# Kernel tuning notes

Measured on AMD Instinct MI355X. Metric: run time of the kernel, lower is better.

## Reference

```python
import jax, jax.numpy as jnp
import numpy as np
from jax import lax

B, W, M = 4, 20, 512
RNN_HID = 64
N_HIDDEN = RNN_HID          # bi = False
HALF = N_HIDDEN // 2
K = 10
LONG_K = W // 2             # conv_long kernel
LONG_OUT = W - 2 * (LONG_K - 1)   # = 2
N_SPATIAL = 10


def setup_inputs() -> dict:
    key = jax.random.key(0)
    ks = jax.random.split(key, 24)
    g = lambda i, shape, s=0.05: jax.random.normal(ks[i], shape, jnp.float32) * s
    return {
        "x": jax.random.normal(ks[0], (B, W, M), jnp.float32),
        # vanilla RNN (tanh), 1 layer, input_size=1
        "W_ih": g(1, (RNN_HID, 1), 0.2), "W_hh": g(2, (RNN_HID, RNN_HID), 0.1),
        "b_ih": g(3, (RNN_HID,)), "b_hh": g(4, (RNN_HID,)),
        # attention adjacency params
        "W1": g(5, (HALF, N_HIDDEN), 0.1), "b1": g(6, (HALF,)),
        "W2": g(7, (HALF, N_HIDDEN), 0.1),
        "V": g(8, (HALF,), 0.1), "bv": g(9, (1,)),
        "Wb": g(10, (M, M), 0.05), "wb": g(11, (1,)),
        # conv / conv_long
        "conv_w": g(12, (K, 1, W), 0.1), "conv_b": g(13, (K,)),
        "convl_w": g(14, (K, 1, LONG_K), 0.1), "convl_b": g(15, (K,)),
        # graph conv layers: adj @ (x @ W) + b
        "gc1_w": g(16, ((1 + LONG_OUT) * K, N_HIDDEN), 0.1), "gc1_b": g(17, (N_HIDDEN,)),
        "gc2_w": g(18, (N_HIDDEN, N_SPATIAL), 0.1), "gc2_b": g(19, (N_SPATIAL,)),
        # output head
        "out_w": g(20, (1, N_HIDDEN + N_SPATIAL), 0.1), "out_b": g(21, (1,)),
        # fixed geographic adjacency (data.adj)
        "adj": jax.random.uniform(ks[22], (M, M), dtype=jnp.float32),
    }


def _conv1d(x, w, b, dilation=1):
    # x: (N, Cin, W), w: (Cout, Cin, K) -> (N, Cout, Wout), VALID padding
    y = lax.conv_general_dilated(x, w, (1,), 'VALID', rhs_dilation=(dilation,),
                                 dimension_numbers=('NCH', 'OIH', 'NCH'))
    return y + b[None, :, None]


def reference(x, W_ih, W_hh, b_ih, b_hh, W1, b1, W2, V, bv, Wb, wb,
              conv_w, conv_b, convl_w, convl_b, gc1_w, gc1_b, gc2_w, gc2_b,
              out_w, out_b, adj):
    b, w, m = x.shape
    # ---- RNN encode each node's scalar series: (b*m, w, 1) -> last hidden ----
    xr = jnp.transpose(x, (0, 2, 1)).reshape(b * m, w)          # (bm, w)
    inp = xr[..., None] @ W_ih.T + b_ih                         # (bm, w, H)

    def step(h, u):
        return jnp.tanh(u + h @ W_hh.T + b_hh), None

    h0 = jnp.zeros((b * m, RNN_HID), x.dtype)
    h_last, _ = lax.scan(step, h0, jnp.swapaxes(inp, 0, 1))     # (bm, H)
    last_hid = h_last.reshape(b, m, N_HIDDEN)
    out_temporal = last_hid

    # ---- pairwise bilinear attention adjacency (broadcast instead of repeat) ----
    p = last_hid @ W1.T                                         # (b, m, H/2)
    q = last_hid @ W2.T                                         # (b, m, H/2)
    e = jax.nn.elu(p[:, :, None, :] + q[:, None, :, :] + b1)    # (b, m, m, H/2)
    a_mx = e @ V + bv[0]                                        # (b, m, m)
    # F.normalize(p=2, dim=1)
    nrm = jnp.maximum(jnp.sqrt(jnp.sum(a_mx * a_mx, axis=1, keepdims=True)), 1e-12)
    a_mx = a_mx / nrm
    c = jax.nn.sigmoid(a_mx @ Wb + wb[0])                       # (b, m, m)
    A = adj[None] * c + a_mx * (1.0 - c)

    # ---- per-node convs, batched over all b*m series (no Python loop) ----
    h_tmp = xr[:, None, :]                                      # (bm, 1, w)
    r = _conv1d(h_tmp, conv_w, conv_b)                          # (bm, k, 1)
    r_long = _conv1d(h_tmp, convl_w, convl_b, dilation=2)       # (bm, k, long_out)
    r_l = jnp.concatenate([r, r_long], axis=-1).reshape(b, m, -1)  # (b, m, (1+lo)*k)
    r_l = jax.nn.relu(r_l)

    # ---- graph convolutions: adj @ (x @ W) + b ----
    xg = jax.nn.relu(A @ (r_l @ gc1_w) + gc1_b)                 # (b, m, H)
    out_spatial = jax.nn.relu(A @ (xg @ gc2_w) + gc2_b)         # (b, m, 10)

    out = jnp.concatenate([out_spatial, out_temporal], axis=-1)
    return (out @ out_w.T + out_b)[..., 0]                      # (b, m)
```

## Files before the change

kernel.cpp:

```cpp
#include <hip/hip_runtime.h>
#include <hip/hip_bf16.h>
#include <cstdint>
#include <cstddef>

#define OFF_P     0
#define OFF_QB    65536
#define OFF_TDOT  131072
#define OFF_COLSQ 133120
#define OFF_ZT    135168
#define OFF_AMXB  155648
#define OFF_ABF   679936
#define OFF_G1T   1204224

typedef __attribute__((ext_vector_type(8))) short short8;
typedef __attribute__((ext_vector_type(8))) unsigned short ushort8;
typedef __attribute__((ext_vector_type(4))) float f32x4;

__device__ inline unsigned short f2bf(float f) {
    unsigned u = __builtin_bit_cast(unsigned, f);
    unsigned r = u + 0x7FFFu + ((u >> 16) & 1u);
    return (unsigned short)(r >> 16);
}
__device__ inline float bf2f(unsigned short s) {
    unsigned u = ((unsigned)s) << 16;
    return __builtin_bit_cast(float, u);
}
__device__ inline float tanh_fast(float x) {
    return 1.f - 2.f/(__expf(2.f*x) + 1.f);
}

__global__ __launch_bounds__(256) void k1_rnn(
    const float* __restrict__ x, const float* __restrict__ W_ih,
    const float* __restrict__ W_hh, const float* __restrict__ b_ih,
    const float* __restrict__ b_hh, const float* __restrict__ W1,
    const float* __restrict__ b1, const float* __restrict__ W2,
    const float* __restrict__ conv_w, const float* __restrict__ conv_b,
    const float* __restrict__ convl_w, const float* __restrict__ convl_b,
    const float* __restrict__ gc1_w, const float* __restrict__ out_w,
    const float* __restrict__ out_b,
    float* __restrict__ p_out, float* __restrict__ qb_out,
    unsigned short* __restrict__ G1T, float* __restrict__ tdot,
    float* __restrict__ colsq)
{
    __shared__ float h_sh[4][64];
    __shared__ float xt_sh[4][20];
    __shared__ float rl_sh[4][30];
    int tid = threadIdx.x;
    int w = tid >> 6, lane = tid & 63;
    int s = blockIdx.x * 4 + w;
    int b = s >> 9, m = s & 511;

    if (blockIdx.x < 8) colsq[blockIdx.x * 256 + tid] = 0.f;

    if (lane < 20) xt_sh[w][lane] = x[(b*20 + lane)*512 + m];

    float wrow[64];
    const float* wr = W_hh + lane*64;
    #pragma unroll
    for (int k4 = 0; k4 < 16; ++k4) {
        float4 v = reinterpret_cast<const float4*>(wr)[k4];
        wrow[4*k4+0]=v.x; wrow[4*k4+1]=v.y; wrow[4*k4+2]=v.z; wrow[4*k4+3]=v.w;
    }
    float wih = W_ih[lane], bih = b_ih[lane], bhh = b_hh[lane];
    h_sh[w][lane] = 0.f;
    float h = 0.f;

    if (lane < 10) {
        float acc = conv_b[lane];
        #pragma unroll
        for (int t = 0; t < 20; ++t) acc += conv_w[lane*20+t]*xt_sh[w][t];
        rl_sh[w][3*lane] = fmaxf(acc, 0.f);
    } else if (lane < 30) {
        int idx = lane-10, j = idx>>1, oo = idx&1;
        float acc = convl_b[j];
        #pragma unroll
        for (int t = 0; t < 10; ++t) acc += convl_w[j*10+t]*xt_sh[w][oo+2*t];
        rl_sh[w][3*j+1+oo] = fmaxf(acc, 0.f);
    }

    for (int t = 0; t < 20; ++t) {
        float acc = xt_sh[w][t]*wih + bih + bhh;
        #pragma unroll
        for (int k = 0; k < 64; ++k) acc += wrow[k]*h_sh[w][k];
        h = tanh_fast(acc);
        h_sh[w][lane] = h;
    }

    float td = h * out_w[10 + lane];
    #pragma unroll
    for (int off = 32; off; off >>= 1) td += __shfl_down(td, off);
    if (lane == 0) tdot[s] = td + out_b[0];

    if (lane < 32) {
        const float* w1r = W1 + lane*64;
        float acc = 0.f;
        #pragma unroll
        for (int k = 0; k < 64; ++k) acc += w1r[k]*h_sh[w][k];
        p_out[s*32 + lane] = acc;
    } else {
        int i = lane - 32;
        const float* w2r = W2 + i*64;
        float acc = 0.f;
        #pragma unroll
        for (int k = 0; k < 64; ++k) acc += w2r[k]*h_sh[w][k];
        qb_out[s*32 + i] = acc + b1[i];
    }

    float g = 0.f;
    #pragma unroll
    for (int t = 0; t < 30; ++t) g += rl_sh[w][t]*gc1_w[t*64 + lane];
    G1T[((size_t)(b*64 + lane))*512 + m] = f2bf(g);
}

__global__ __launch_bounds__(256) void k2_amx(
    const float* __restrict__ p, const float* __restrict__ qb,
    const float* __restrict__ V, const float* __restrict__ bv,
    unsigned short* __restrict__ amxB, float* __restrict__ colsq)
{
    __shared__ float p_sh[32*36], q_sh[32*36], v_sh[32], sq_sh[32*17];
    int t = threadIdx.x;
    int b = blockIdx.z, i0 = blockIdx.y*32, j0 = blockIdx.x*32;
    {
        int r = t >> 3, c4 = (t & 7)*4;
        *(float4*)&p_sh[r*36 + c4] = *(const float4*)(p  + (size_t)(b*512 + i0 + r)*32 + c4);
        *(float4*)&q_sh[r*36 + c4] = *(const float4*)(qb + (size_t)(b*512 + j0 + r)*32 + c4);
    }
    if (t < 32) v_sh[t] = V[t];
    __syncthreads();

    int ti = t >> 4, tj = t & 15;
    float bv0 = bv[0];
    float a00 = bv0, a01 = bv0, a10 = bv0, a11 = bv0;
    #pragma unroll
    for (int h = 0; h < 32; ++h) {
        float p0 = p_sh[ti*36 + h], p1 = p_sh[(ti+16)*36 + h];
        float q0 = q_sh[tj*36 + h], q1 = q_sh[(tj+16)*36 + h];
        float vh = v_sh[h];
        float x00 = p0+q0, x01 = p0+q1, x10 = p1+q0, x11 = p1+q1;
        float e00 = x00 > 0.f ? x00 : __expf(x00)-1.f;
        float e01 = x01 > 0.f ? x01 : __expf(x01)-1.f;
        float e10 = x10 > 0.f ? x10 : __expf(x10)-1.f;
        float e11 = x11 > 0.f ? x11 : __expf(x11)-1.f;
        a00 += vh*e00; a01 += vh*e01; a10 += vh*e10; a11 += vh*e11;
    }
    size_t base0 = ((size_t)(b*512 + i0 + ti))*512 + j0;
    size_t base1 = ((size_t)(b*512 + i0 + ti + 16))*512 + j0;
    amxB[base0 + tj]      = f2bf(a00);
    amxB[base0 + tj + 16] = f2bf(a01);
    amxB[base1 + tj]      = f2bf(a10);
    amxB[base1 + tj + 16] = f2bf(a11);

    sq_sh[tj*17 + ti]      = a00*a00 + a10*a10;
    sq_sh[(tj+16)*17 + ti] = a01*a01 + a11*a11;
    __syncthreads();
    if (t < 32) {
        float ssum = 0.f;
        #pragma unroll
        for (int r = 0; r < 16; ++r) ssum += sq_sh[t*17 + r];
        atomicAdd(&colsq[b*512 + j0 + t], ssum);
    }
}

__global__ __launch_bounds__(64) void k3a_mfma(
    const unsigned short* __restrict__ amxB, const float* __restrict__ Wb,
    const float* __restrict__ colsq, const float* __restrict__ wb,
    const float* __restrict__ adj, unsigned short* __restrict__ Abf)
{
    int lane = threadIdx.x;
    int b = blockIdx.z;
    int i0 = blockIdx.y*32, j0 = blockIdx.x*32;
    f32x4 acc[2][2] = {};

    int kslice = (lane>>4)*8;
    int fr = lane & 15;
    const unsigned short* abase = amxB + ((size_t)(b*512 + i0 + fr))*512 + kslice;
    const float* wcol = Wb + j0 + fr;
    const float* csq  = colsq + b*512 + kslice;

    for (int k0 = 0; k0 < 512; k0 += 32) {
        float4 c0 = *(const float4*)(csq + k0);
        float4 c1 = *(const float4*)(csq + k0 + 4);
        float inv[8] = {
            rsqrtf(fmaxf(c0.x,1e-24f)), rsqrtf(fmaxf(c0.y,1e-24f)),
            rsqrtf(fmaxf(c0.z,1e-24f)), rsqrtf(fmaxf(c0.w,1e-24f)),
            rsqrtf(fmaxf(c1.x,1e-24f)), rsqrtf(fmaxf(c1.y,1e-24f)),
            rsqrtf(fmaxf(c1.z,1e-24f)), rsqrtf(fmaxf(c1.w,1e-24f)) };

        short8 a0 = *(const short8*)(abase + k0);
        short8 a1 = *(const short8*)(abase + 16*512 + k0);

        const float* wk = wcol + (size_t)(k0 + kslice)*512;
        short8 b0, b1;
        #pragma unroll
        for (int m = 0; m < 8; ++m) {
            b0[m] = (short)f2bf(wk[(size_t)m*512]      * inv[m]);
            b1[m] = (short)f2bf(wk[(size_t)m*512 + 16] * inv[m]);
        }

        acc[0][0] = __builtin_amdgcn_mfma_f32_16x16x32_bf16(a0, b0, acc[0][0],0,0,0);
        acc[0][1] = __builtin_amdgcn_mfma_f32_16x16x32_bf16(a0, b1, acc[0][1],0,0,0);
        acc[1][0] = __builtin_amdgcn_mfma_f32_16x16x32_bf16(a1, b0, acc[1][0],0,0,0);
        acc[1][1] = __builtin_amdgcn_mfma_f32_16x16x32_bf16(a1, b1, acc[1][1],0,0,0);
    }

    float wbs = wb[0];
    #pragma unroll
    for (int fj = 0; fj < 2; ++fj) {
        int j = j0 + fj*16 + fr;
        float inv = rsqrtf(fmaxf(colsq[b*512 + j], 1e-24f));
        #pragma unroll
        for (int fi = 0; fi < 2; ++fi)
        #pragma unroll
        for (int r = 0; r < 4; ++r) {
            int i = i0 + fi*16 + (lane>>4)*4 + r;
            float S = acc[fi][fj][r] + wbs;
            float c = 1.f/(1.f + __expf(-S));
            float aN = bf2f(amxB[((size_t)(b*512)+i)*512 + j]) * inv;
            Abf[((size_t)(b*512)+i)*512 + j] = f2bf(adj[i*512+j]*c + aN*(1.f - c));
        }
    }
}

#define AS_STRIDE 520
__global__ __launch_bounds__(256) void k3b_mfma(
    const unsigned short* __restrict__ Abf, const unsigned short* __restrict__ G1T,
    const float* __restrict__ gc1_b, const float* __restrict__ gc2_w,
    float* __restrict__ zT)
{
    __shared__ __align__(16) unsigned short As[16*AS_STRIDE];
    __shared__ float xg[16][68];
    int t = threadIdx.x;
    int b = blockIdx.y, i0 = blockIdx.x*16;
    int wv = t >> 6, lane = t & 63;

    {
        int r = t >> 4, seg = (t & 15)*32;
        const unsigned short* src = Abf + ((size_t)(b*512 + i0 + r))*512 + seg;
        *(short8*)&As[r*AS_STRIDE + seg]      = *(const short8*)src;
        *(short8*)&As[r*AS_STRIDE + seg + 8]  = *(const short8*)(src + 8);
        *(short8*)&As[r*AS_STRIDE + seg + 16] = *(const short8*)(src + 16);
        *(short8*)&As[r*AS_STRIDE + seg + 24] = *(const short8*)(src + 24);
    }
    __syncthreads();

    f32x4 acc = {};
    const unsigned short* gbase = G1T + ((size_t)(b*64 + wv*16 + (lane&15)))*512 + (lane>>4)*8;
    int aoff = (lane&15)*AS_STRIDE + (lane>>4)*8;
    #pragma unroll 4
    for (int k0 = 0; k0 < 512; k0 += 32) {
        short8 af = *(const short8*)&As[aoff + k0];
        short8 bf = *(const short8*)(gbase + k0);
        acc = __builtin_amdgcn_mfma_f32_16x16x32_bf16(af, bf, acc, 0,0,0);
    }

    {
        int cc = wv*16 + (lane&15);
        float gb = gc1_b[cc];
        #pragma unroll
        for (int r = 0; r < 4; ++r)
            xg[(lane>>4)*4 + r][cc] = fmaxf(acc[r] + gb, 0.f);
    }
    __syncthreads();

    if (t < 160) {
        int row = t/10, sx = t%10;
        float a = 0.f;
        #pragma unroll
        for (int c = 0; c < 64; ++c) a += xg[row][c]*gc2_w[c*10 + sx];
        zT[((size_t)(b*10) + sx)*512 + i0 + row] = a;
    }
}

__global__ __launch_bounds__(256) void k4_out(
    const unsigned short* __restrict__ Abf, const float* __restrict__ zT,
    const float* __restrict__ gc2_b, const float* __restrict__ out_w,
    const float* __restrict__ tdot, float* __restrict__ out)
{
    int t = threadIdx.x;
    int w = t >> 6, lane = t & 63;
    int s = blockIdx.x*4 + w;
    int b = s >> 9;

    short8 av = *(const short8*)(Abf + (size_t)s*512 + lane*8);
    float a[8];
    #pragma unroll
    for (int q = 0; q < 8; ++q) a[q] = bf2f((unsigned short)av[q]);

    float acc[10];
    #pragma unroll
    for (int sx = 0; sx < 10; ++sx) {
        const float* zr = zT + ((size_t)(b*10) + sx)*512 + lane*8;
        float4 z0 = *(const float4*)zr;
        float4 z1 = *(const float4*)(zr + 4);
        acc[sx] = a[0]*z0.x + a[1]*z0.y + a[2]*z0.z + a[3]*z0.w
                + a[4]*z1.x + a[5]*z1.y + a[6]*z1.z + a[7]*z1.w;
    }
    #pragma unroll
    for (int sx = 0; sx < 10; ++sx)
        #pragma unroll
        for (int off = 32; off; off >>= 1) acc[sx] += __shfl_down(acc[sx], off);
    if (lane == 0) {
        float o = tdot[s];
        #pragma unroll
        for (int sx = 0; sx < 10; ++sx)
            o += fmaxf(acc[sx] + gc2_b[sx], 0.f) * out_w[sx];
        out[s] = o;
    }
}

extern "C" void kernel_launch(void* const* d_in, const int* in_sizes, int n_in,
                              void* d_out, int out_size, void* d_ws, size_t ws_size,
                              hipStream_t stream) {
    const float* x       = (const float*)d_in[0];
    const float* W_ih    = (const float*)d_in[1];
    const float* W_hh    = (const float*)d_in[2];
    const float* b_ih    = (const float*)d_in[3];
    const float* b_hh    = (const float*)d_in[4];
    const float* W1      = (const float*)d_in[5];
    const float* b1      = (const float*)d_in[6];
    const float* W2      = (const float*)d_in[7];
    const float* V       = (const float*)d_in[8];
    const float* bv      = (const float*)d_in[9];
    const float* Wb      = (const float*)d_in[10];
    const float* wb      = (const float*)d_in[11];
    const float* conv_w  = (const float*)d_in[12];
    const float* conv_b  = (const float*)d_in[13];
    const float* convl_w = (const float*)d_in[14];
    const float* convl_b = (const float*)d_in[15];
    const float* gc1_w   = (const float*)d_in[16];
    const float* gc1_b   = (const float*)d_in[17];
    const float* gc2_w   = (const float*)d_in[18];
    const float* gc2_b   = (const float*)d_in[19];
    const float* out_w   = (const float*)d_in[20];
    const float* out_b   = (const float*)d_in[21];
    const float* adj     = (const float*)d_in[22];

    float* ws    = (float*)d_ws;
    float* p     = ws + OFF_P;
    float* qb    = ws + OFF_QB;
    float* tdot  = ws + OFF_TDOT;
    float* colsq = ws + OFF_COLSQ;
    float* zT    = ws + OFF_ZT;
    unsigned short* amxB = (unsigned short*)(ws + OFF_AMXB);
    unsigned short* Abf  = (unsigned short*)(ws + OFF_ABF);
    unsigned short* G1T  = (unsigned short*)(ws + OFF_G1T);
    float* out   = (float*)d_out;

    k1_rnn<<<dim3(512), dim3(256), 0, stream>>>(
        x, W_ih, W_hh, b_ih, b_hh, W1, b1, W2,
        conv_w, conv_b, convl_w, convl_b, gc1_w, out_w, out_b,
        p, qb, G1T, tdot, colsq);

    k2_amx<<<dim3(16,16,4), dim3(256), 0, stream>>>(p, qb, V, bv, amxB, colsq);

    k3a_mfma<<<dim3(16,16,4), dim3(64), 0, stream>>>(amxB, Wb, colsq, wb, adj, Abf);
    k3b_mfma<<<dim3(32,4), dim3(256), 0, stream>>>(Abf, G1T, gc1_b, gc2_w, zT);
    k4_out<<<dim3(512), dim3(256), 0, stream>>>(Abf, zT, gc2_b, out_w, tdot, out);
}
```

Baseline: 59.42 us.

## Fuse gate GEMM with first graph-conv GEMM and pre-transpose Wb to bf16

Merges k3a and k3b into one kernel. Each block loads a 16-row strip of the attention matrix, normalizes it once into LDS, computes the gate GEMM against a bf16 transposed Wb, writes the blended adjacency to both global memory and LDS, then runs the G1 GEMM straight from LDS. Wb is transposed and converted to bf16 in extra blocks of the RNN kernel. This removes one launch, re-reading Abf, and the per-k fp32 Wb conversion inside the MFMA loop. The cost is only 128 blocks doing a full 16x512x512 GEMM each, which lowers parallelism. Normalization is now applied to A in bf16 rather than folded into the fp32 B operand, so rounding changes slightly.

```diff
diff --git a/kernel.cpp b/kernel.cpp
--- a/kernel.cpp
+++ b/kernel.cpp
@@ -11,6 +11,7 @@
 #define OFF_AMXB  155648
 #define OFF_ABF   679936
 #define OFF_G1T   1204224
+#define OFF_WBT   1269760
 
 typedef __attribute__((ext_vector_type(8))) short short8;
 typedef __attribute__((ext_vector_type(8))) unsigned short ushort8;
@@ -37,15 +38,40 @@
     const float* __restrict__ conv_w, const float* __restrict__ conv_b,
     const float* __restrict__ convl_w, const float* __restrict__ convl_b,
     const float* __restrict__ gc1_w, const float* __restrict__ out_w,
-    const float* __restrict__ out_b,
+    const float* __restrict__ out_b, const float* __restrict__ Wb,
     float* __restrict__ p_out, float* __restrict__ qb_out,
     unsigned short* __restrict__ G1T, float* __restrict__ tdot,
-    float* __restrict__ colsq)
+    float* __restrict__ colsq, unsigned short* __restrict__ WbT)
 {
     __shared__ float h_sh[4][64];
     __shared__ float xt_sh[4][20];
     __shared__ float rl_sh[4][30];
+    __shared__ float tile[64][68];
     int tid = threadIdx.x;
+
+    if (blockIdx.x >= 512) {
+        int tt = blockIdx.x - 512;
+        int k0 = (tt >> 3) * 64, j0 = (tt & 7) * 64;
+        #pragma unroll
+        for (int q = 0; q < 4; ++q) {
+            int kr = (tid>>4) + 16*q;
+            int jc = (tid&15)*4;
+            *(float4*)&tile[kr][jc] = *(const float4*)(Wb + (size_t)(k0+kr)*512 + j0 + jc);
+        }
+        __syncthreads();
+        int jl = tid>>2, kc = (tid&3)*16;
+        int j = j0 + jl;
+        ushort8 v0, v1;
+        #pragma unroll
+        for (int kk = 0; kk < 8; ++kk) v0[kk] = f2bf(tile[kc+kk][jl]);
+        #pragma unroll
+        for (int kk = 0; kk < 8; ++kk) v1[kk] = f2bf(tile[kc+8+kk][jl]);
+        unsigned short* dst = WbT + (size_t)j*512 + k0 + kc;
+        *(ushort8*)dst = v0;
+        *(ushort8*)(dst+8) = v1;
+        return;
+    }
+
     int w = tid >> 6, lane = tid & 63;
     int s = blockIdx.x * 4 + w;
     int b = s >> 9, m = s & 511;
@@ -161,104 +187,90 @@
     }
 }
 
-__global__ __launch_bounds__(64) void k3a_mfma(
-    const unsigned short* __restrict__ amxB, const float* __restrict__ Wb,
-    const float* __restrict__ colsq, const float* __restrict__ wb,
-    const float* __restrict__ adj, unsigned short* __restrict__ Abf)
+#define K3S 520
+__global__ __launch_bounds__(256) void k3_fused(
+    const unsigned short* __restrict__ amxB, const unsigned short* __restrict__ WbT,
+    const unsigned short* __restrict__ G1T, const float* __restrict__ colsq,
+    const float* __restrict__ wb, const float* __restrict__ adj,
+    const float* __restrict__ gc1_b, const float* __restrict__ gc2_w,
+    unsigned short* __restrict__ Abf, float* __restrict__ zT)
 {
-    int lane = threadIdx.x;
-    int b = blockIdx.z;
-    int i0 = blockIdx.y*32, j0 = blockIdx.x*32;
-    f32x4 acc[2][2] = {};
-
-    int kslice = (lane>>4)*8;
-    int fr = lane & 15;
-    const unsigned short* abase = amxB + ((size_t)(b*512 + i0 + fr))*512 + kslice;
-    const float* wcol = Wb + j0 + fr;
-    const float* csq  = colsq + b*512 + kslice;
-
-    for (int k0 = 0; k0 < 512; k0 += 32) {
-        float4 c0 = *(const float4*)(csq + k0);
-        float4 c1 = *(const float4*)(csq + k0 + 4);
-        float inv[8] = {
-            rsqrtf(fmaxf(c0.x,1e-24f)), rsqrtf(fmaxf(c0.y,1e-24f)),
-            rsqrtf(fmaxf(c0.z,1e-24f)), rsqrtf(fmaxf(c0.w,1e-24f)),
-            rsqrtf(fmaxf(c1.x,1e-24f)), rsqrtf(fmaxf(c1.y,1e-24f)),
-            rsqrtf(fmaxf(c1.z,1e-24f)), rsqrtf(fmaxf(c1.w,1e-24f)) };
-
-        short8 a0 = *(const short8*)(abase + k0);
-        short8 a1 = *(const short8*)(abase + 16*512 + k0);
-
-        const float* wk = wcol + (size_t)(k0 + kslice)*512;
-        short8 b0, b1;
-        #pragma unroll
-        for (int m = 0; m < 8; ++m) {
-            b0[m] = (short)f2bf(wk[(size_t)m*512]      * inv[m]);
-            b1[m] = (short)f2bf(wk[(size_t)m*512 + 16] * inv[m]);
-        }
-
-        acc[0][0] = __builtin_amdgcn_mfma_f32_16x16x32_bf16(a0, b0, acc[0][0],0,0,0);
-        acc[0][1] = __builtin_amdgcn_mfma_f32_16x16x32_bf16(a0, b1, acc[0][1],0,0,0);
-        acc[1][0] = __builtin_amdgcn_mfma_f32_16x16x32_bf16(a1, b0, acc[1][0],0,0,0);
-        acc[1][1] = __builtin_amdgcn_mfma_f32_16x16x32_bf16(a1, b1, acc[1][1],0,0,0);
-    }
-
-    float wbs = wb[0];
-    #pragma unroll
-    for (int fj = 0; fj < 2; ++fj) {
-        int j = j0 + fj*16 + fr;
-        float inv = rsqrtf(fmaxf(colsq[b*512 + j], 1e-24f));
-        #pragma unroll
-        for (int fi = 0; fi < 2; ++fi)
-        #pragma unroll
-        for (int r = 0; r < 4; ++r) {
-            int i = i0 + fi*16 + (lane>>4)*4 + r;
-            float S = acc[fi][fj][r] + wbs;
-            float c = 1.f/(1.f + __expf(-S));
-            float aN = bf2f(amxB[((size_t)(b*512)+i)*512 + j]) * inv;
-            Abf[((size_t)(b*512)+i)*512 + j] = f2bf(adj[i*512+j]*c + aN*(1.f - c));
-        }
-    }
-}
-
-#define AS_STRIDE 520
-__global__ __launch_bounds__(256) void k3b_mfma(
-    const unsigned short* __restrict__ Abf, const unsigned short* __restrict__ G1T,
-    const float* __restrict__ gc1_b, const float* __restrict__ gc2_w,
-    float* __restrict__ zT)
-{
-    __shared__ __align__(16) unsigned short As[16*AS_STRIDE];
+    __shared__ float inv_lds[512];
+    __shared__ __align__(16) unsigned short A_lds[16*K3S];
     __shared__ float xg[16][68];
     int t = threadIdx.x;
     int b = blockIdx.y, i0 = blockIdx.x*16;
     int wv = t >> 6, lane = t & 63;
+    int fr = lane & 15, sl = (lane>>4)*8;
+
+    if (t < 128) {
+        float4 c = *(const float4*)(colsq + b*512 + t*4);
+        float4 iv = { rsqrtf(fmaxf(c.x,1e-24f)), rsqrtf(fmaxf(c.y,1e-24f)),
+                      rsqrtf(fmaxf(c.z,1e-24f)), rsqrtf(fmaxf(c.w,1e-24f)) };
+        *(float4*)&inv_lds[t*4] = iv;
+    }
+    __syncthreads();
 
     {
         int r = t >> 4, seg = (t & 15)*32;
-        const unsigned short* src = Abf + ((size_t)(b*512 + i0 + r))*512 + seg;
-        *(short8*)&As[r*AS_STRIDE + seg]      = *(const short8*)src;
-        *(short8*)&As[r*AS_STRIDE + seg + 8]  = *(const short8*)(src + 8);
-        *(short8*)&As[r*AS_STRIDE + seg + 16] = *(const short8*)(src + 16);
-        *(short8*)&As[r*AS_STRIDE + seg + 24] = *(const short8*)(src + 24);
-    }
-    __syncthreads();
-
-    f32x4 acc = {};
-    const unsigned short* gbase = G1T + ((size_t)(b*64 + wv*16 + (lane&15)))*512 + (lane>>4)*8;
-    int aoff = (lane&15)*AS_STRIDE + (lane>>4)*8;
-    #pragma unroll 4
+        const unsigned short* src = amxB + ((size_t)(b*512 + i0 + r))*512 + seg;
+        #pragma unroll
+        for (int q = 0; q < 4; ++q) {
+            short8 v = *(const short8*)(src + q*8);
+            ushort8 o;
+            #pragma unroll
+            for (int e = 0; e < 8; ++e)
+                o[e] = f2bf(bf2f((unsigned short)v[e]) * inv_lds[seg + q*8 + e]);
+            *(ushort8*)&A_lds[r*K3S + seg + q*8] = o;
+        }
+    }
+    __syncthreads();
+
+    f32x4 acc[8] = {};
+    int wj0 = wv*128;
     for (int k0 = 0; k0 < 512; k0 += 32) {
-        short8 af = *(const short8*)&As[aoff + k0];
-        short8 bf = *(const short8*)(gbase + k0);
-        acc = __builtin_amdgcn_mfma_f32_16x16x32_bf16(af, bf, acc, 0,0,0);
-    }
+        short8 a = *(const short8*)&A_lds[fr*K3S + k0 + sl];
+        #pragma unroll
+        for (int fj = 0; fj < 8; ++fj) {
+            short8 bb = *(const short8*)(WbT + ((size_t)(wj0 + fj*16 + fr))*512 + k0 + sl);
+            acc[fj] = __builtin_amdgcn_mfma_f32_16x16x32_bf16(a, bb, acc[fj],0,0,0);
+        }
+    }
+    __syncthreads();
 
     {
-        int cc = wv*16 + (lane&15);
+        float wbs = wb[0];
+        #pragma unroll
+        for (int fj = 0; fj < 8; ++fj) {
+            int j = wj0 + fj*16 + fr;
+            #pragma unroll
+            for (int r = 0; r < 4; ++r) {
+                int i = sl/2 + r;
+                float S = acc[fj][r] + wbs;
+                float c = 1.f/(1.f + __expf(-S));
+                float aN = bf2f(A_lds[i*K3S + j]);
+                unsigned short u = f2bf(adj[(size_t)(i0+i)*512 + j]*c + aN*(1.f - c));
+                Abf[((size_t)(b*512) + i0 + i)*512 + j] = u;
+                A_lds[i*K3S + j] = u;
+            }
+        }
+    }
+    __syncthreads();
+
+    {
+        f32x4 acc2 = {};
+        const unsigned short* gbase = G1T + ((size_t)(b*64 + wv*16 + fr))*512 + sl;
+        #pragma unroll 4
+        for (int k0 = 0; k0 < 512; k0 += 32) {
+            short8 a = *(const short8*)&A_lds[fr*K3S + k0 + sl];
+            short8 g = *(const short8*)(gbase + k0);
+            acc2 = __builtin_amdgcn_mfma_f32_16x16x32_bf16(a, g, acc2,0,0,0);
+        }
+        int cc = wv*16 + fr;
         float gb = gc1_b[cc];
         #pragma unroll
         for (int r = 0; r < 4; ++r)
-            xg[(lane>>4)*4 + r][cc] = fmaxf(acc[r] + gb, 0.f);
+            xg[sl/2 + r][cc] = fmaxf(acc2[r] + gb, 0.f);
     }
     __syncthreads();
 
@@ -344,16 +356,18 @@
     unsigned short* amxB = (unsigned short*)(ws + OFF_AMXB);
     unsigned short* Abf  = (unsigned short*)(ws + OFF_ABF);
     unsigned short* G1T  = (unsigned short*)(ws + OFF_G1T);
+    unsigned short* WbT  = (unsigned short*)(ws + OFF_WBT);
     float* out   = (float*)d_out;
 
-    k1_rnn<<<dim3(512), dim3(256), 0, stream>>>(
+    k1_rnn<<<dim3(576), dim3(256), 0, stream>>>(
         x, W_ih, W_hh, b_ih, b_hh, W1, b1, W2,
-        conv_w, conv_b, convl_w, convl_b, gc1_w, out_w, out_b,
-        p, qb, G1T, tdot, colsq);
+        conv_w, conv_b, convl_w, convl_b, gc1_w, out_w, out_b, Wb,
+        p, qb, G1T, tdot, colsq, WbT);
 
     k2_amx<<<dim3(16,16,4), dim3(256), 0, stream>>>(p, qb, V, bv, amxB, colsq);
 
-    k3a_mfma<<<dim3(16,16,4), dim3(64), 0, stream>>>(amxB, Wb, colsq, wb, adj, Abf);
-    k3b_mfma<<<dim3(32,4), dim3(256), 0, stream>>>(Abf, G1T, gc1_b, gc2_w, zT);
+    k3_fused<<<dim3(32,4), dim3(256), 0, stream>>>(
+        amxB, WbT, G1T, colsq, wb, adj, gc1_b, gc2_w, Abf, zT);
+
     k4_out<<<dim3(512), dim3(256), 0, stream>>>(Abf, zT, gc2_b, out_w, tdot, out);
 }
```

Result: slower. 80.59 us (+35.6%).

## Pre-transpose Wb to bf16 in RNN kernel and apply norm scaling on A side

Applied to the files above, without the earlier changes.

Adds 64 extra blocks to the RNN kernel that transpose Wb into a bf16 k-contiguous layout in workspace. The Wb GEMM kernel then loads B fragments as vectors instead of eight strided fp32 loads with per-element conversion. The column-norm scaling moves onto the amx operand, which is now bf16-decoded, scaled and re-rounded. The RNN recurrence inner product is also split into four accumulators to shorten the dependency chain, at the cost of extra shared-memory use in the RNN kernel and a slightly different rounding path.

```diff
diff --git a/kernel.cpp b/kernel.cpp
--- a/kernel.cpp
+++ b/kernel.cpp
@@ -11,6 +11,7 @@
 #define OFF_AMXB  155648
 #define OFF_ABF   679936
 #define OFF_G1T   1204224
+#define OFF_WBT   1269760
 
 typedef __attribute__((ext_vector_type(8))) short short8;
 typedef __attribute__((ext_vector_type(8))) unsigned short ushort8;
@@ -37,15 +38,40 @@
     const float* __restrict__ conv_w, const float* __restrict__ conv_b,
     const float* __restrict__ convl_w, const float* __restrict__ convl_b,
     const float* __restrict__ gc1_w, const float* __restrict__ out_w,
-    const float* __restrict__ out_b,
+    const float* __restrict__ out_b, const float* __restrict__ Wb,
     float* __restrict__ p_out, float* __restrict__ qb_out,
     unsigned short* __restrict__ G1T, float* __restrict__ tdot,
-    float* __restrict__ colsq)
+    float* __restrict__ colsq, unsigned short* __restrict__ WbT)
 {
     __shared__ float h_sh[4][64];
     __shared__ float xt_sh[4][20];
     __shared__ float rl_sh[4][30];
+    __shared__ float tile[64][68];
     int tid = threadIdx.x;
+
+    if (blockIdx.x >= 512) {
+        int tt = blockIdx.x - 512;
+        int k0 = (tt >> 3) * 64, j0 = (tt & 7) * 64;
+        #pragma unroll
+        for (int q = 0; q < 4; ++q) {
+            int kr = (tid>>4) + 16*q;
+            int jc = (tid&15)*4;
+            *(float4*)&tile[kr][jc] = *(const float4*)(Wb + (size_t)(k0+kr)*512 + j0 + jc);
+        }
+        __syncthreads();
+        int jl = tid>>2, kc = (tid&3)*16;
+        int j = j0 + jl;
+        ushort8 v0, v1;
+        #pragma unroll
+        for (int kk = 0; kk < 8; ++kk) v0[kk] = f2bf(tile[kc+kk][jl]);
+        #pragma unroll
+        for (int kk = 0; kk < 8; ++kk) v1[kk] = f2bf(tile[kc+8+kk][jl]);
+        unsigned short* dst = WbT + (size_t)j*512 + k0 + kc;
+        *(ushort8*)dst = v0;
+        *(ushort8*)(dst+8) = v1;
+        return;
+    }
+
     int w = tid >> 6, lane = tid & 63;
     int s = blockIdx.x * 4 + w;
     int b = s >> 9, m = s & 511;
@@ -79,9 +105,15 @@
     }
 
     for (int t = 0; t < 20; ++t) {
-        float acc = xt_sh[w][t]*wih + bih + bhh;
-        #pragma unroll
-        for (int k = 0; k < 64; ++k) acc += wrow[k]*h_sh[w][k];
+        float a0=0.f, a1=0.f, a2=0.f, a3=0.f;
+        #pragma unroll
+        for (int k = 0; k < 64; k += 4) {
+            a0 += wrow[k+0]*h_sh[w][k+0];
+            a1 += wrow[k+1]*h_sh[w][k+1];
+            a2 += wrow[k+2]*h_sh[w][k+2];
+            a3 += wrow[k+3]*h_sh[w][k+3];
+        }
+        float acc = xt_sh[w][t]*wih + bih + bhh + ((a0+a1)+(a2+a3));
         h = tanh_fast(acc);
         h_sh[w][lane] = h;
     }
@@ -162,7 +194,7 @@
 }
 
 __global__ __launch_bounds__(64) void k3a_mfma(
-    const unsigned short* __restrict__ amxB, const float* __restrict__ Wb,
+    const unsigned short* __restrict__ amxB, const unsigned short* __restrict__ WbT,
     const float* __restrict__ colsq, const float* __restrict__ wb,
     const float* __restrict__ adj, unsigned short* __restrict__ Abf)
 {
@@ -171,30 +203,32 @@
     int i0 = blockIdx.y*32, j0 = blockIdx.x*32;
     f32x4 acc[2][2] = {};
 
-    int kslice = (lane>>4)*8;
+    int sl = (lane>>4)*8;
     int fr = lane & 15;
-    const unsigned short* abase = amxB + ((size_t)(b*512 + i0 + fr))*512 + kslice;
-    const float* wcol = Wb + j0 + fr;
-    const float* csq  = colsq + b*512 + kslice;
-
+    const unsigned short* abase = amxB + ((size_t)(b*512 + i0 + fr))*512 + sl;
+    const unsigned short* bbase = WbT  + ((size_t)(j0 + fr))*512 + sl;
+    const float* csq = colsq + b*512 + sl;
+
+    #pragma unroll 2
     for (int k0 = 0; k0 < 512; k0 += 32) {
         float4 c0 = *(const float4*)(csq + k0);
         float4 c1 = *(const float4*)(csq + k0 + 4);
-        float inv[8] = {
+        float iv[8] = {
             rsqrtf(fmaxf(c0.x,1e-24f)), rsqrtf(fmaxf(c0.y,1e-24f)),
             rsqrtf(fmaxf(c0.z,1e-24f)), rsqrtf(fmaxf(c0.w,1e-24f)),
             rsqrtf(fmaxf(c1.x,1e-24f)), rsqrtf(fmaxf(c1.y,1e-24f)),
             rsqrtf(fmaxf(c1.z,1e-24f)), rsqrtf(fmaxf(c1.w,1e-24f)) };
 
-        short8 a0 = *(const short8*)(abase + k0);
-        short8 a1 = *(const short8*)(abase + 16*512 + k0);
-
-        const float* wk = wcol + (size_t)(k0 + kslice)*512;
-        short8 b0, b1;
-        #pragma unroll
-        for (int m = 0; m < 8; ++m) {
-            b0[m] = (short)f2bf(wk[(size_t)m*512]      * inv[m]);
-            b1[m] = (short)f2bf(wk[(size_t)m*512 + 16] * inv[m]);
+        short8 a0r = *(const short8*)(abase + k0);
+        short8 a1r = *(const short8*)(abase + 16*512 + k0);
+        short8 b0  = *(const short8*)(bbase + k0);
+        short8 b1  = *(const short8*)(bbase + 16*512 + k0);
+
+        short8 a0, a1;
+        #pragma unroll
+        for (int e = 0; e < 8; ++e) {
+            a0[e] = (short)f2bf(bf2f((unsigned short)a0r[e]) * iv[e]);
+            a1[e] = (short)f2bf(bf2f((unsigned short)a1r[e]) * iv[e]);
         }
 
         acc[0][0] = __builtin_amdgcn_mfma_f32_16x16x32_bf16(a0, b0, acc[0][0],0,0,0);
@@ -344,16 +378,19 @@
     unsigned short* amxB = (unsigned short*)(ws + OFF_AMXB);
     unsigned short* Abf  = (unsigned short*)(ws + OFF_ABF);
     unsigned short* G1T  = (unsigned short*)(ws + OFF_G1T);
+    unsigned short* WbT  = (unsigned short*)(ws + OFF_WBT);
     float* out   = (float*)d_out;
 
-    k1_rnn<<<dim3(512), dim3(256), 0, stream>>>(
+    k1_rnn<<<dim3(576), dim3(256), 0, stream>>>(
         x, W_ih, W_hh, b_ih, b_hh, W1, b1, W2,
-        conv_w, conv_b, convl_w, convl_b, gc1_w, out_w, out_b,
-        p, qb, G1T, tdot, colsq);
+        conv_w, conv_b, convl_w, convl_b, gc1_w, out_w, out_b, Wb,
+        p, qb, G1T, tdot, colsq, WbT);
 
     k2_amx<<<dim3(16,16,4), dim3(256), 0, stream>>>(p, qb, V, bv, amxB, colsq);
 
-    k3a_mfma<<<dim3(16,16,4), dim3(64), 0, stream>>>(amxB, Wb, colsq, wb, adj, Abf);
+    k3a_mfma<<<dim3(16,16,4), dim3(64), 0, stream>>>(amxB, WbT, colsq, wb, adj, Abf);
+
     k3b_mfma<<<dim3(32,4), dim3(256), 0, stream>>>(Abf, G1T, gc1_b, gc2_w, zT);
+
     k4_out<<<dim3(512), dim3(256), 0, stream>>>(Abf, zT, gc2_b, out_w, tdot, out);
 }
```

Result: slower. 61.04 us (+2.7%).
